# Performance work log

Hardware: AMD Instinct MI355X
Metric: run time of the kernel (lower is better)

The kernel has to match this reference:

```python
import jax, jax.numpy as jnp
import numpy as np

N_AGENTS = 3
OBS_DIM = 30
ACT_DIM = 9
HIDDEN = 128
HEADS = 4
HEAD_DIM = HIDDEN // HEADS
BATCH = 131072
NEG_SLOPE = 0.01
MASK_VAL = -1e10


def _leaky(x):
    return jnp.where(x >= 0, x, NEG_SLOPE * x)


def setup_inputs() -> dict:
    key = jax.random.key(0)
    ks = jax.random.split(key, 20)

    def init(k, shape, fan_in):
        return jax.random.normal(k, shape, dtype=jnp.float32) / np.sqrt(fan_in)

    inp = {
        "observations": jax.random.normal(ks[0], (BATCH, N_AGENTS, OBS_DIM), dtype=jnp.float32),
        "actions": jax.random.uniform(ks[1], (BATCH, N_AGENTS, ACT_DIM), dtype=jnp.float32),
        # per-agent embed weights, stacked over agents: [N, in, out] (already transposed vs torch)
        "W_o": init(ks[2], (N_AGENTS, OBS_DIM, HIDDEN), OBS_DIM),
        "b_o": jnp.zeros((N_AGENTS, HIDDEN), dtype=jnp.float32),
        "W_oa": init(ks[3], (N_AGENTS, OBS_DIM + ACT_DIM, HIDDEN), OBS_DIM + ACT_DIM),
        "b_oa": jnp.zeros((N_AGENTS, HIDDEN), dtype=jnp.float32),
        # shared attention projections: [in, out]
        "Wq": init(ks[4], (HIDDEN, HIDDEN), HIDDEN),
        "bq": jnp.zeros((HIDDEN,), dtype=jnp.float32),
        "Wk": init(ks[5], (HIDDEN, HIDDEN), HIDDEN),
        "bk": jnp.zeros((HIDDEN,), dtype=jnp.float32),
        "Wv": init(ks[6], (HIDDEN, HIDDEN), HIDDEN),
        "bv": jnp.zeros((HIDDEN,), dtype=jnp.float32),
        # per-agent critic MLP: Linear(2H->H) + LeakyReLU + Linear(H->A)
        "Wc1": init(ks[7], (N_AGENTS, 2 * HIDDEN, HIDDEN), 2 * HIDDEN),
        "bc1": jnp.zeros((N_AGENTS, HIDDEN), dtype=jnp.float32),
        "Wc2": init(ks[8], (N_AGENTS, HIDDEN, ACT_DIM), HIDDEN),
        "bc2": jnp.zeros((N_AGENTS, ACT_DIM), dtype=jnp.float32),
    }
    return inp


def reference(observations, actions, W_o, b_o, W_oa, b_oa, Wq, bq, Wk, bk, Wv, bv, Wc1, bc1, Wc2, bc2):
    B, N, _ = observations.shape

    # per-agent embeds as a single batched GEMM over the agent axis
    o_emb = _leaky(jnp.einsum('bnd,ndh->bnh', observations, W_o) + b_o)          # [B,N,H]
    oa = jnp.concatenate([observations, actions], axis=-1)                        # [B,N,O+A]
    oa_emb = _leaky(jnp.einsum('bnd,ndh->bnh', oa, W_oa) + b_oa)                  # [B,N,H]

    # shared Q/K/V projections, split heads -> [B, heads, N, head_dim]
    def heads(x):
        return x.reshape(B, N, HEADS, HEAD_DIM).transpose(0, 2, 1, 3)

    Q = heads(o_emb @ Wq + bq)
    K = heads(oa_emb @ Wk + bk)
    V = heads(oa_emb @ Wv + bv)

    scores = jnp.einsum('bhnd,bhmd->bhnm', Q, K) / np.sqrt(HEAD_DIM).astype(np.float32)
    mask = jnp.where(jnp.eye(N, dtype=bool), jnp.float32(MASK_VAL), 0.0)          # diag masked
    attn = jax.nn.softmax(scores + mask, axis=-1)
    attn_out = jnp.einsum('bhnm,bhmd->bhnd', attn, V)
    attn_out = attn_out.transpose(0, 2, 1, 3).reshape(B, N, HIDDEN)               # [B,N,H]

    # per-agent critics, again batched over the agent axis
    c_in = jnp.concatenate([o_emb, attn_out], axis=-1)                            # [B,N,2H]
    h = _leaky(jnp.einsum('bnd,ndh->bnh', c_in, Wc1) + bc1)
    q_values = jnp.einsum('bnh,nha->bna', h, Wc2) + bc2                           # [B,N,A]
    return q_values
```

## Files before the change

kernel.cpp:

```cpp
#include <hip/hip_runtime.h>
#include <stdint.h>

typedef unsigned short u16;
typedef unsigned int u32;
typedef __attribute__((ext_vector_type(8))) short short8;
typedef __attribute__((ext_vector_type(4))) float floatx4;

#define BATCH   131072
#define NA      3
#define OBS     30
#define ACTD    9
#define HID     128
#define HEADS   4
#define HD      32
#define MB      16
#define ROWS    (MB*NA)
#define LDC     136
#define LDOA    72
#define QSCALE  0.17677669529663687f
#define NTHREADS 512

#define OFF_WO    0
#define OFF_WOA   12288
#define OFF_WQ    36864
#define OFF_WK    53248
#define OFF_WV    69632
#define OFF_WC1   86016
#define OFF_WC2   184320
#define PRE_TOTAL 190464

__device__ __forceinline__ u16 f2bf(float f) {
    union { float f; u32 u; } v; v.f = f;
    return (u16)((v.u + 0x8000u) >> 16);
}
__device__ __forceinline__ u32 pk_bf16(float a, float b) {
    union { float f; u32 u; } x, y; x.f = a; y.f = b;
    return ((x.u + 0x8000u) >> 16) | ((y.u + 0x8000u) & 0xffff0000u);
}
__device__ __forceinline__ float lo16f(u32 w) { union { u32 u; float f; } v; v.u = w << 16; return v.f; }
__device__ __forceinline__ float hi16f(u32 w) { union { u32 u; float f; } v; v.u = w & 0xffff0000u; return v.f; }
__device__ __forceinline__ float leaky(float x) { return x >= 0.f ? x : 0.01f * x; }

__global__ void prepack_kernel(const float* __restrict__ Wo,  const float* __restrict__ Woa,
                               const float* __restrict__ Wq,  const float* __restrict__ Wk,
                               const float* __restrict__ Wv,  const float* __restrict__ Wc1,
                               const float* __restrict__ Wc2, u16* __restrict__ out) {
    int i = blockIdx.x * blockDim.x + threadIdx.x;
    if (i >= PRE_TOTAL) return;
    const float* src; int K, KT, perA, base, Nsrc, Nlim; float scl = 1.f;
    if (i < OFF_WOA)      { src = Wo;  K = 30;  KT = 1; perA = 4096;  base = OFF_WO;  Nsrc = 128; Nlim = 128; }
    else if (i < OFF_WQ)  { src = Woa; K = 39;  KT = 2; perA = 8192;  base = OFF_WOA; Nsrc = 128; Nlim = 128; }
    else if (i < OFF_WK)  { src = Wq;  K = 128; KT = 4; perA = 16384; base = OFF_WQ;  Nsrc = 128; Nlim = 128; scl = QSCALE; }
    else if (i < OFF_WV)  { src = Wk;  K = 128; KT = 4; perA = 16384; base = OFF_WK;  Nsrc = 128; Nlim = 128; }
    else if (i < OFF_WC1) { src = Wv;  K = 128; KT = 4; perA = 16384; base = OFF_WV;  Nsrc = 128; Nlim = 128; }
    else if (i < OFF_WC2) { src = Wc1; K = 256; KT = 8; perA = 32768; base = OFF_WC1; Nsrc = 128; Nlim = 128; }
    else                  { src = Wc2; K = 128; KT = 4; perA = 2048;  base = OFF_WC2; Nsrc = 9;   Nlim = 9;   }
    int j = i - base;
    int agent = j / perA;
    int r = j - agent * perA;
    int e = r & 7, lane = (r >> 3) & 63, fk = r >> 9;
    int kt = fk % KT, nt = fk / KT;
    int n = nt * 16 + (lane & 15);
    int k = kt * 32 + (lane >> 4) * 8 + e;
    u16 v = 0;
    if (k < K && n < Nlim) v = f2bf(src[(agent * K + k) * Nsrc + n] * scl);
    out[i] = v;
}

__global__ __launch_bounds__(NTHREADS, 6) void fused_kernel(
    const float* __restrict__ obs, const float* __restrict__ act,
    const float* __restrict__ b_o, const float* __restrict__ b_oa,
    const float* __restrict__ bq,  const float* __restrict__ bk_, const float* __restrict__ bv,
    const float* __restrict__ bc1, const float* __restrict__ bc2,
    const u16* __restrict__ pre, float* __restrict__ out)
{
    __shared__ __align__(16) u16 s_mem[4 * ROWS * LDC];
    u16* s_oemb  = s_mem;
    u16* s_oaemb = s_mem + ROWS * LDC;
    u16* s_bufA  = s_mem + 2 * ROWS * LDC;
    u16* s_bufB  = s_mem + 3 * ROWS * LDC;

    const int tid  = threadIdx.x;
    const int wave = tid >> 6, lane = tid & 63;
    const int l15  = lane & 15, quad = lane >> 4;
    const int b0   = blockIdx.x * MB;
    const short8* preV = (const short8*)pre;

    for (int g = tid; g < ROWS * 15; g += NTHREADS) {
        int r = g / 15, s = g - r * 15;
        int n = r / MB, bl = r - n * MB;
        const float* src = &obs[((b0 + bl) * NA + n) * OBS + 2 * s];
        *(u32*)&s_bufA[n * (MB * LDOA) + bl * LDOA + 2 * s] = pk_bf16(src[0], src[1]);
    }
    for (int g = tid; g < ROWS * 5; g += NTHREADS) {
        int r = g / 5, s = g - r * 5;
        int n = r / MB, bl = r - n * MB;
        const float* src = &act[((b0 + bl) * NA + n) * ACTD + 2 * s];
        float v0 = src[0], v1 = (s < 4) ? src[1] : 0.f;
        *(u32*)&s_bufA[n * (MB * LDOA) + bl * LDOA + 30 + 2 * s] = pk_bf16(v0, v1);
    }
    for (int g = tid; g < ROWS * 12; g += NTHREADS) {
        int r = g / 12, s = g - r * 12;
        int n = r / MB, bl = r - n * MB;
        *(u32*)&s_bufA[n * (MB * LDOA) + bl * LDOA + 40 + 2 * s] = 0;
    }
    __syncthreads();

    for (int sj = wave; sj < 24; sj += 8) {
        int osel = sj / 12;
        int rem = sj % 12, agent = rem >> 2, nh2 = rem & 3;
        int KTn = osel ? 2 : 1;
        const float* bias = osel ? b_oa : b_o;
        int preBase = osel ? (OFF_WOA / 8 + agent * 1024) : (OFF_WO / 8 + agent * 512);
        floatx4 acc[2] = {};
        for (int kt = 0; kt < KTn; kt++) {
            short8 a = *(const short8*)&s_bufA[agent * (MB * LDOA) + l15 * LDOA + kt * 32 + quad * 8];
            #pragma unroll
            for (int n2 = 0; n2 < 2; n2++) {
                int nt = nh2 * 2 + n2;
                short8 b = preV[preBase + (nt * KTn + kt) * 64 + lane];
                acc[n2] = __builtin_amdgcn_mfma_f32_16x16x32_bf16(a, b, acc[n2], 0, 0, 0);
            }
        }
        u16* dst = osel ? s_oaemb : s_oemb;
        #pragma unroll
        for (int n2 = 0; n2 < 2; n2++) {
            int col = (nh2 * 2 + n2) * 16 + l15;
            float bb = bias[agent * HID + col];
            #pragma unroll
            for (int rg = 0; rg < 4; rg++) {
                int m = quad * 4 + rg;
                dst[(m * NA + agent) * LDC + col] = f2bf(leaky(acc[n2][rg] + bb));
            }
        }
    }
    __syncthreads();

    {
        int proj = wave >> 2, nh2 = wave & 3;
        const u16* Abuf = proj ? s_oaemb : s_oemb;
        int preBase = (proj ? OFF_WK : OFF_WQ) / 8;
        u16* dst = proj ? s_bufB : s_bufA;
        const float* bias = proj ? bk_ : bq;
        float bscl = proj ? 1.f : QSCALE;
        short8 wf[8];
        #pragma unroll
        for (int n2 = 0; n2 < 2; n2++)
            #pragma unroll
            for (int kt = 0; kt < 4; kt++)
                wf[n2 * 4 + kt] = preV[preBase + ((nh2 * 2 + n2) * 4 + kt) * 64 + lane];
        for (int mt = 0; mt < 3; mt++) {
            short8 xa[4];
            #pragma unroll
            for (int kt = 0; kt < 4; kt++)
                xa[kt] = *(const short8*)&Abuf[(mt * 16 + l15) * LDC + kt * 32 + quad * 8];
            floatx4 acc[2] = {};
            #pragma unroll
            for (int n2 = 0; n2 < 2; n2++)
                #pragma unroll
                for (int kt = 0; kt < 4; kt++)
                    acc[n2] = __builtin_amdgcn_mfma_f32_16x16x32_bf16(xa[kt], wf[n2 * 4 + kt], acc[n2], 0, 0, 0);
            #pragma unroll
            for (int n2 = 0; n2 < 2; n2++) {
                int col = (nh2 * 2 + n2) * 16 + l15;
                float bb = bias[col] * bscl;
                #pragma unroll
                for (int rg = 0; rg < 4; rg++) {
                    int m = mt * 16 + quad * 4 + rg;
                    dst[m * LDC + col] = f2bf(acc[n2][rg] + bb);
                }
            }
        }
    }
    __syncthreads();

    float2 prob = make_float2(0.f, 0.f);
    int e3 = 0, h3 = 0, n3 = 0, m30 = 0, m31 = 0;
    const bool attn_thread = (tid < MB * HEADS * NA);
    if (attn_thread) {
        int r = tid;
        e3 = r / (HEADS * NA); r -= e3 * HEADS * NA; h3 = r / NA; n3 = r - h3 * NA;
        m30 = (n3 == 0) ? 1 : 0;
        m31 = (n3 == 2) ? 1 : 2;
        const uint4* qp  = (const uint4*)&s_bufA[(e3 * NA + n3) * LDC + h3 * HD];
        const uint4* kp0 = (const uint4*)&s_bufB[(e3 * NA + m30) * LDC + h3 * HD];
        const uint4* kp1 = (const uint4*)&s_bufB[(e3 * NA + m31) * LDC + h3 * HD];
        float s0 = 0.f, s1 = 0.f;
        #pragma unroll
        for (int c = 0; c < 4; c++) {
            uint4 qw = qp[c], aw = kp0[c], bw = kp1[c];
            u32 qv[4] = {qw.x, qw.y, qw.z, qw.w};
            u32 av[4] = {aw.x, aw.y, aw.z, aw.w};
            u32 bv_[4] = {bw.x, bw.y, bw.z, bw.w};
            #pragma unroll
            for (int j = 0; j < 4; j++) {
                float ql = lo16f(qv[j]), qh = hi16f(qv[j]);
                s0 += ql * lo16f(av[j]) + qh * hi16f(av[j]);
                s1 += ql * lo16f(bv_[j]) + qh * hi16f(bv_[j]);
            }
        }
        float mx = fmaxf(s0, s1);
        float p0 = __expf(s0 - mx), p1 = __expf(s1 - mx);
        float inv = 1.f / (p0 + p1);
        prob = make_float2(p0 * inv, p1 * inv);
    }
    __syncthreads();

    {
        int nt = wave;
        short8 wf[4];
        #pragma unroll
        for (int kt = 0; kt < 4; kt++)
            wf[kt] = preV[OFF_WV / 8 + (nt * 4 + kt) * 64 + lane];
        for (int mt = 0; mt < 3; mt++) {
            short8 xa[4];
            #pragma unroll
            for (int kt = 0; kt < 4; kt++)
                xa[kt] = *(const short8*)&s_oaemb[(mt * 16 + l15) * LDC + kt * 32 + quad * 8];
            floatx4 acc = {};
            #pragma unroll
            for (int kt = 0; kt < 4; kt++)
                acc = __builtin_amdgcn_mfma_f32_16x16x32_bf16(xa[kt], wf[kt], acc, 0, 0, 0);
            int col = nt * 16 + l15;
            float bb = bv[col];
            #pragma unroll
            for (int rg = 0; rg < 4; rg++) {
                int m = mt * 16 + quad * 4 + rg;
                s_bufA[m * LDC + col] = f2bf(acc[rg] + bb);
            }
        }
    }
    __syncthreads();

    if (attn_thread) {
        const uint4* v0p = (const uint4*)&s_bufA[(e3 * NA + m30) * LDC + h3 * HD];
        const uint4* v1p = (const uint4*)&s_bufA[(e3 * NA + m31) * LDC + h3 * HD];
        uint4* dst = (uint4*)&s_oaemb[(e3 * NA + n3) * LDC + h3 * HD];
        #pragma unroll
        for (int c = 0; c < 4; c++) {
            uint4 aw = v0p[c], bw = v1p[c], ow;
            u32 av[4] = {aw.x, aw.y, aw.z, aw.w};
            u32 bv_[4] = {bw.x, bw.y, bw.z, bw.w};
            u32 ov[4];
            #pragma unroll
            for (int j = 0; j < 4; j++) {
                float lo = prob.x * lo16f(av[j]) + prob.y * lo16f(bv_[j]);
                float hi = prob.x * hi16f(av[j]) + prob.y * hi16f(bv_[j]);
                ov[j] = pk_bf16(lo, hi);
            }
            ow.x = ov[0]; ow.y = ov[1]; ow.z = ov[2]; ow.w = ov[3];
            dst[c] = ow;
        }
    }
    __syncthreads();

    for (int sj = wave; sj < 24; sj += 8) {
        int agent = sj >> 3, nt = sj & 7;
        floatx4 acc = {};
        for (int kt = 0; kt < 8; kt++) {
            const u16* A = (kt < 4) ? s_oemb : s_oaemb;
            int kk = (kt & 3) * 32 + quad * 8;
            short8 a = *(const short8*)&A[(l15 * NA + agent) * LDC + kk];
            short8 b = preV[OFF_WC1 / 8 + agent * 4096 + (nt * 8 + kt) * 64 + lane];
            acc = __builtin_amdgcn_mfma_f32_16x16x32_bf16(a, b, acc, 0, 0, 0);
        }
        int col = nt * 16 + l15;
        float bb = bc1[agent * HID + col];
        #pragma unroll
        for (int rg = 0; rg < 4; rg++) {
            int m = quad * 4 + rg;
            s_bufB[(m * NA + agent) * LDC + col] = f2bf(leaky(acc[rg] + bb));
        }
    }
    __syncthreads();

    if (wave < NA) {
        int agent = wave;
        floatx4 acc = {};
        #pragma unroll
        for (int kt = 0; kt < 4; kt++) {
            short8 a = *(const short8*)&s_bufB[(l15 * NA + agent) * LDC + kt * 32 + quad * 8];
            short8 b = preV[OFF_WC2 / 8 + agent * 256 + kt * 64 + lane];
            acc = __builtin_amdgcn_mfma_f32_16x16x32_bf16(a, b, acc, 0, 0, 0);
        }
        int col = l15;
        if (col < ACTD) {
            float bb = bc2[agent * ACTD + col];
            #pragma unroll
            for (int rg = 0; rg < 4; rg++) {
                int m = quad * 4 + rg;
                out[((b0 + m) * NA + agent) * ACTD + col] = acc[rg] + bb;
            }
        }
    }
}

extern "C" void kernel_launch(void* const* d_in, const int* in_sizes, int n_in,
                              void* d_out, int out_size, void* d_ws, size_t ws_size,
                              hipStream_t stream) {
    const float* obs = (const float*)d_in[0];
    const float* act = (const float*)d_in[1];
    const float* Wo  = (const float*)d_in[2];
    const float* bo  = (const float*)d_in[3];
    const float* Woa = (const float*)d_in[4];
    const float* boa = (const float*)d_in[5];
    const float* Wq  = (const float*)d_in[6];
    const float* bq  = (const float*)d_in[7];
    const float* Wk  = (const float*)d_in[8];
    const float* bk  = (const float*)d_in[9];
    const float* Wv  = (const float*)d_in[10];
    const float* bv  = (const float*)d_in[11];
    const float* Wc1 = (const float*)d_in[12];
    const float* bc1 = (const float*)d_in[13];
    const float* Wc2 = (const float*)d_in[14];
    const float* bc2 = (const float*)d_in[15];
    u16* pre = (u16*)d_ws;

    prepack_kernel<<<(PRE_TOTAL + 255) / 256, 256, 0, stream>>>(Wo, Woa, Wq, Wk, Wv, Wc1, Wc2, pre);
    fused_kernel<<<BATCH / MB, NTHREADS, 0, stream>>>(obs, act, bo, boa, bq, bk, bv, bc1, bc2, pre,
                                                      (float*)d_out);
}
```

Measured before the change: 261.6 us.

## Prefetch weight fragments into registers ahead of each GEMM stage

Global loads of the per-stage bf16 weight fragments and biases are hoisted ahead of earlier stages and barriers (embed and Q/K weights at kernel start, V weights after input staging, Wc1 after the Q/K projection, Wc2 before the critic layer). This hides global-memory latency behind the LDS staging and preceding compute. The zero-fill loop also switches to 16-byte stores. The cost is much higher register pressure, e.g. 24 short8 for Wc1 alone held across stages, which can lower occupancy or cause spills at 512 threads per block.

```diff
diff --git a/kernel.cpp b/kernel.cpp
--- a/kernel.cpp
+++ b/kernel.cpp
@@ -86,6 +86,40 @@
     const int b0   = blockIdx.x * MB;
     const short8* preV = (const short8*)pre;
 
+    short8 w1[3][2][2]; float b1v[3][2];
+    int os1[3], ag1[3], nh21[3], ktn1[3];
+    #pragma unroll
+    for (int j = 0; j < 3; j++) {
+        int sj = wave + 8 * j;
+        int osel = sj / 12;
+        int rem = sj % 12, agent = rem >> 2, nh2 = rem & 3;
+        int KTn = osel ? 2 : 1;
+        int preBase = osel ? (OFF_WOA / 8 + agent * 1024) : (OFF_WO / 8 + agent * 512);
+        const float* bias = osel ? b_oa : b_o;
+        os1[j] = osel; ag1[j] = agent; nh21[j] = nh2; ktn1[j] = KTn;
+        #pragma unroll
+        for (int n2 = 0; n2 < 2; n2++) {
+            int nt = nh2 * 2 + n2;
+            w1[j][n2][0] = preV[preBase + (nt * KTn + 0) * 64 + lane];
+            if (KTn == 2) w1[j][n2][1] = preV[preBase + (nt * KTn + 1) * 64 + lane];
+            b1v[j][n2] = bias[agent * HID + nt * 16 + l15];
+        }
+    }
+    short8 w2[8]; float b2v[2];
+    {
+        int proj = wave >> 2, nh2s = wave & 3;
+        int preBase = (proj ? OFF_WK : OFF_WQ) / 8;
+        const float* bias = proj ? bk_ : bq;
+        float bscl = proj ? 1.f : QSCALE;
+        #pragma unroll
+        for (int n2 = 0; n2 < 2; n2++) {
+            b2v[n2] = bias[(nh2s * 2 + n2) * 16 + l15] * bscl;
+            #pragma unroll
+            for (int kt = 0; kt < 4; kt++)
+                w2[n2 * 4 + kt] = preV[preBase + ((nh2s * 2 + n2) * 4 + kt) * 64 + lane];
+        }
+    }
+
     for (int g = tid; g < ROWS * 15; g += NTHREADS) {
         int r = g / 15, s = g - r * 15;
         int n = r / MB, bl = r - n * MB;
@@ -99,34 +133,38 @@
         float v0 = src[0], v1 = (s < 4) ? src[1] : 0.f;
         *(u32*)&s_bufA[n * (MB * LDOA) + bl * LDOA + 30 + 2 * s] = pk_bf16(v0, v1);
     }
-    for (int g = tid; g < ROWS * 12; g += NTHREADS) {
-        int r = g / 12, s = g - r * 12;
+    for (int g = tid; g < ROWS * 3; g += NTHREADS) {
+        int r = g / 3, s = g - r * 3;
         int n = r / MB, bl = r - n * MB;
-        *(u32*)&s_bufA[n * (MB * LDOA) + bl * LDOA + 40 + 2 * s] = 0;
-    }
-    __syncthreads();
-
-    for (int sj = wave; sj < 24; sj += 8) {
-        int osel = sj / 12;
-        int rem = sj % 12, agent = rem >> 2, nh2 = rem & 3;
-        int KTn = osel ? 2 : 1;
-        const float* bias = osel ? b_oa : b_o;
-        int preBase = osel ? (OFF_WOA / 8 + agent * 1024) : (OFF_WO / 8 + agent * 512);
+        *(uint4*)&s_bufA[n * (MB * LDOA) + bl * LDOA + 40 + 8 * s] = make_uint4(0, 0, 0, 0);
+    }
+    __syncthreads();
+
+    short8 w3[4]; float b3v;
+    {
+        #pragma unroll
+        for (int kt = 0; kt < 4; kt++)
+            w3[kt] = preV[OFF_WV / 8 + (wave * 4 + kt) * 64 + lane];
+        b3v = bv[wave * 16 + l15];
+    }
+
+    #pragma unroll
+    for (int j = 0; j < 3; j++) {
+        int osel = os1[j], agent = ag1[j], nh2 = nh21[j], KTn = ktn1[j];
         floatx4 acc[2] = {};
-        for (int kt = 0; kt < KTn; kt++) {
-            short8 a = *(const short8*)&s_bufA[agent * (MB * LDOA) + l15 * LDOA + kt * 32 + quad * 8];
-            #pragma unroll
-            for (int n2 = 0; n2 < 2; n2++) {
-                int nt = nh2 * 2 + n2;
-                short8 b = preV[preBase + (nt * KTn + kt) * 64 + lane];
-                acc[n2] = __builtin_amdgcn_mfma_f32_16x16x32_bf16(a, b, acc[n2], 0, 0, 0);
+        #pragma unroll
+        for (int kt = 0; kt < 2; kt++) {
+            if (kt < KTn) {
+                short8 a = *(const short8*)&s_bufA[agent * (MB * LDOA) + l15 * LDOA + kt * 32 + quad * 8];
+                acc[0] = __builtin_amdgcn_mfma_f32_16x16x32_bf16(a, w1[j][0][kt], acc[0], 0, 0, 0);
+                acc[1] = __builtin_amdgcn_mfma_f32_16x16x32_bf16(a, w1[j][1][kt], acc[1], 0, 0, 0);
             }
         }
         u16* dst = osel ? s_oaemb : s_oemb;
         #pragma unroll
         for (int n2 = 0; n2 < 2; n2++) {
             int col = (nh2 * 2 + n2) * 16 + l15;
-            float bb = bias[agent * HID + col];
+            float bb = b1v[j][n2];
             #pragma unroll
             for (int rg = 0; rg < 4; rg++) {
                 int m = quad * 4 + rg;
@@ -139,16 +177,7 @@
     {
         int proj = wave >> 2, nh2 = wave & 3;
         const u16* Abuf = proj ? s_oaemb : s_oemb;
-        int preBase = (proj ? OFF_WK : OFF_WQ) / 8;
         u16* dst = proj ? s_bufB : s_bufA;
-        const float* bias = proj ? bk_ : bq;
-        float bscl = proj ? 1.f : QSCALE;
-        short8 wf[8];
-        #pragma unroll
-        for (int n2 = 0; n2 < 2; n2++)
-            #pragma unroll
-            for (int kt = 0; kt < 4; kt++)
-                wf[n2 * 4 + kt] = preV[preBase + ((nh2 * 2 + n2) * 4 + kt) * 64 + lane];
         for (int mt = 0; mt < 3; mt++) {
             short8 xa[4];
             #pragma unroll
@@ -159,11 +188,11 @@
             for (int n2 = 0; n2 < 2; n2++)
                 #pragma unroll
                 for (int kt = 0; kt < 4; kt++)
-                    acc[n2] = __builtin_amdgcn_mfma_f32_16x16x32_bf16(xa[kt], wf[n2 * 4 + kt], acc[n2], 0, 0, 0);
+                    acc[n2] = __builtin_amdgcn_mfma_f32_16x16x32_bf16(xa[kt], w2[n2 * 4 + kt], acc[n2], 0, 0, 0);
             #pragma unroll
             for (int n2 = 0; n2 < 2; n2++) {
                 int col = (nh2 * 2 + n2) * 16 + l15;
-                float bb = bias[col] * bscl;
+                float bb = b2v[n2];
                 #pragma unroll
                 for (int rg = 0; rg < 4; rg++) {
                     int m = mt * 16 + quad * 4 + rg;
@@ -173,6 +202,15 @@
         }
     }
     __syncthreads();
+
+    short8 w4[3][8]; float b4v[3];
+    #pragma unroll
+    for (int j = 0; j < 3; j++) {
+        #pragma unroll
+        for (int kt = 0; kt < 8; kt++)
+            w4[j][kt] = preV[OFF_WC1 / 8 + j * 4096 + (wave * 8 + kt) * 64 + lane];
+        b4v[j] = bc1[j * HID + wave * 16 + l15];
+    }
 
     float2 prob = make_float2(0.f, 0.f);
     int e3 = 0, h3 = 0, n3 = 0, m30 = 0, m31 = 0;
@@ -208,10 +246,6 @@
 
     {
         int nt = wave;
-        short8 wf[4];
-        #pragma unroll
-        for (int kt = 0; kt < 4; kt++)
-            wf[kt] = preV[OFF_WV / 8 + (nt * 4 + kt) * 64 + lane];
         for (int mt = 0; mt < 3; mt++) {
             short8 xa[4];
             #pragma unroll
@@ -220,9 +254,9 @@
             floatx4 acc = {};
             #pragma unroll
             for (int kt = 0; kt < 4; kt++)
-                acc = __builtin_amdgcn_mfma_f32_16x16x32_bf16(xa[kt], wf[kt], acc, 0, 0, 0);
+                acc = __builtin_amdgcn_mfma_f32_16x16x32_bf16(xa[kt], w3[kt], acc, 0, 0, 0);
             int col = nt * 16 + l15;
-            float bb = bv[col];
+            float bb = b3v;
             #pragma unroll
             for (int rg = 0; rg < 4; rg++) {
                 int m = mt * 16 + quad * 4 + rg;
@@ -254,18 +288,27 @@
     }
     __syncthreads();
 
-    for (int sj = wave; sj < 24; sj += 8) {
-        int agent = sj >> 3, nt = sj & 7;
+    short8 w5[4]; float b5v = 0.f;
+    if (wave < NA) {
+        #pragma unroll
+        for (int kt = 0; kt < 4; kt++)
+            w5[kt] = preV[OFF_WC2 / 8 + wave * 256 + kt * 64 + lane];
+        if (l15 < ACTD) b5v = bc2[wave * ACTD + l15];
+    }
+
+    #pragma unroll
+    for (int j = 0; j < 3; j++) {
+        int agent = j, nt = wave;
         floatx4 acc = {};
+        #pragma unroll
         for (int kt = 0; kt < 8; kt++) {
             const u16* A = (kt < 4) ? s_oemb : s_oaemb;
             int kk = (kt & 3) * 32 + quad * 8;
             short8 a = *(const short8*)&A[(l15 * NA + agent) * LDC + kk];
-            short8 b = preV[OFF_WC1 / 8 + agent * 4096 + (nt * 8 + kt) * 64 + lane];
-            acc = __builtin_amdgcn_mfma_f32_16x16x32_bf16(a, b, acc, 0, 0, 0);
+            acc = __builtin_amdgcn_mfma_f32_16x16x32_bf16(a, w4[j][kt], acc, 0, 0, 0);
         }
         int col = nt * 16 + l15;
-        float bb = bc1[agent * HID + col];
+        float bb = b4v[j];
         #pragma unroll
         for (int rg = 0; rg < 4; rg++) {
             int m = quad * 4 + rg;
@@ -280,16 +323,14 @@
         #pragma unroll
         for (int kt = 0; kt < 4; kt++) {
             short8 a = *(const short8*)&s_bufB[(l15 * NA + agent) * LDC + kt * 32 + quad * 8];
-            short8 b = preV[OFF_WC2 / 8 + agent * 256 + kt * 64 + lane];
-            acc = __builtin_amdgcn_mfma_f32_16x16x32_bf16(a, b, acc, 0, 0, 0);
+            acc = __builtin_amdgcn_mfma_f32_16x16x32_bf16(a, w5[kt], acc, 0, 0, 0);
         }
         int col = l15;
         if (col < ACTD) {
-            float bb = bc2[agent * ACTD + col];
             #pragma unroll
             for (int rg = 0; rg < 4; rg++) {
                 int m = quad * 4 + rg;
-                out[((b0 + m) * NA + agent) * ACTD + col] = acc[rg] + bb;
+                out[((b0 + m) * NA + agent) * ACTD + col] = acc[rg] + b5v;
             }
         }
     }
```

Result: slower. 897.4 us (+243.0%).

## Prefetch all stage weights into registers ahead of each barrier phase

Applied to the files above, without the earlier changes.

Weight and bias fragments for every GEMM stage (embeds, Q/K, V, critic layer 1, critic layer 2) are now loaded from global memory into registers one phase early, so their latency overlaps the input staging, the attention math and the barrier waits. The embedding and critic stages are restructured with a fixed per-wave assignment, so each wave handles its three jobs with the weights already in hand. The padding-zero fill also switches to 16-byte stores. The cost is much higher register pressure, mostly from the 24 short8 critic weight fragments, which may lower occupancy or cause spills.

```diff
diff --git a/kernel.cpp b/kernel.cpp
--- a/kernel.cpp
+++ b/kernel.cpp
@@ -28,6 +28,8 @@
 #define OFF_WC1   86016
 #define OFF_WC2   184320
 #define PRE_TOTAL 190464
+
+#define MFMA(A,B,C) __builtin_amdgcn_mfma_f32_16x16x32_bf16((A),(B),(C),0,0,0)
 
 __device__ __forceinline__ u16 f2bf(float f) {
     union { float f; u32 u; } v; v.f = f;
@@ -86,6 +88,49 @@
     const int b0   = blockIdx.x * MB;
     const short8* preV = (const short8*)pre;
 
+    const int nh2 = wave & 3;
+
+    const int ag0 = wave >> 2;
+    const int ag2 = (wave + 4) >> 2;
+    const int pb0 = OFF_WO / 8 + ag0 * 512;
+    const int pb1 = (wave < 4) ? (OFF_WO / 8 + 2 * 512) : (OFF_WOA / 8);
+    const int kt1n = (wave < 4) ? 1 : 2;
+    const int pb2 = OFF_WOA / 8 + ag2 * 1024;
+    short8 w1_00 = preV[pb0 + (nh2 * 2 + 0) * 64 + lane];
+    short8 w1_01 = preV[pb0 + (nh2 * 2 + 1) * 64 + lane];
+    short8 w1_100 = preV[pb1 + ((nh2 * 2 + 0) * kt1n + 0) * 64 + lane];
+    short8 w1_101 = preV[pb1 + ((nh2 * 2 + 0) * kt1n + 1) * 64 + lane];
+    short8 w1_110 = preV[pb1 + ((nh2 * 2 + 1) * kt1n + 0) * 64 + lane];
+    short8 w1_111 = preV[pb1 + ((nh2 * 2 + 1) * kt1n + 1) * 64 + lane];
+    short8 w1_200 = preV[pb2 + ((nh2 * 2 + 0) * 2 + 0) * 64 + lane];
+    short8 w1_201 = preV[pb2 + ((nh2 * 2 + 0) * 2 + 1) * 64 + lane];
+    short8 w1_210 = preV[pb2 + ((nh2 * 2 + 1) * 2 + 0) * 64 + lane];
+    short8 w1_211 = preV[pb2 + ((nh2 * 2 + 1) * 2 + 1) * 64 + lane];
+    const float* bj0 = b_o + ag0 * HID;
+    const float* bj1 = (wave < 4) ? (b_o + 2 * HID) : b_oa;
+    const float* bj2 = b_oa + ag2 * HID;
+    float b1_00 = bj0[(nh2 * 2 + 0) * 16 + l15];
+    float b1_01 = bj0[(nh2 * 2 + 1) * 16 + l15];
+    float b1_10 = bj1[(nh2 * 2 + 0) * 16 + l15];
+    float b1_11 = bj1[(nh2 * 2 + 1) * 16 + l15];
+    float b1_20 = bj2[(nh2 * 2 + 0) * 16 + l15];
+    float b1_21 = bj2[(nh2 * 2 + 1) * 16 + l15];
+
+    const int proj = wave >> 2;
+    const int pbqk = (proj ? OFF_WK : OFF_WQ) / 8;
+    const float* bqk = proj ? bk_ : bq;
+    const float bscl = proj ? 1.f : QSCALE;
+    short8 w2_00 = preV[pbqk + ((nh2 * 2 + 0) * 4 + 0) * 64 + lane];
+    short8 w2_01 = preV[pbqk + ((nh2 * 2 + 0) * 4 + 1) * 64 + lane];
+    short8 w2_02 = preV[pbqk + ((nh2 * 2 + 0) * 4 + 2) * 64 + lane];
+    short8 w2_03 = preV[pbqk + ((nh2 * 2 + 0) * 4 + 3) * 64 + lane];
+    short8 w2_10 = preV[pbqk + ((nh2 * 2 + 1) * 4 + 0) * 64 + lane];
+    short8 w2_11 = preV[pbqk + ((nh2 * 2 + 1) * 4 + 1) * 64 + lane];
+    short8 w2_12 = preV[pbqk + ((nh2 * 2 + 1) * 4 + 2) * 64 + lane];
+    short8 w2_13 = preV[pbqk + ((nh2 * 2 + 1) * 4 + 3) * 64 + lane];
+    float b2_0 = bqk[(nh2 * 2 + 0) * 16 + l15] * bscl;
+    float b2_1 = bqk[(nh2 * 2 + 1) * 16 + l15] * bscl;
+
     for (int g = tid; g < ROWS * 15; g += NTHREADS) {
         int r = g / 15, s = g - r * 15;
         int n = r / MB, bl = r - n * MB;
@@ -99,80 +144,121 @@
         float v0 = src[0], v1 = (s < 4) ? src[1] : 0.f;
         *(u32*)&s_bufA[n * (MB * LDOA) + bl * LDOA + 30 + 2 * s] = pk_bf16(v0, v1);
     }
-    for (int g = tid; g < ROWS * 12; g += NTHREADS) {
-        int r = g / 12, s = g - r * 12;
+    for (int g = tid; g < ROWS * 3; g += NTHREADS) {
+        int r = g / 3, s = g - r * 3;
         int n = r / MB, bl = r - n * MB;
-        *(u32*)&s_bufA[n * (MB * LDOA) + bl * LDOA + 40 + 2 * s] = 0;
-    }
-    __syncthreads();
-
-    for (int sj = wave; sj < 24; sj += 8) {
-        int osel = sj / 12;
-        int rem = sj % 12, agent = rem >> 2, nh2 = rem & 3;
-        int KTn = osel ? 2 : 1;
-        const float* bias = osel ? b_oa : b_o;
-        int preBase = osel ? (OFF_WOA / 8 + agent * 1024) : (OFF_WO / 8 + agent * 512);
-        floatx4 acc[2] = {};
-        for (int kt = 0; kt < KTn; kt++) {
-            short8 a = *(const short8*)&s_bufA[agent * (MB * LDOA) + l15 * LDOA + kt * 32 + quad * 8];
-            #pragma unroll
-            for (int n2 = 0; n2 < 2; n2++) {
-                int nt = nh2 * 2 + n2;
-                short8 b = preV[preBase + (nt * KTn + kt) * 64 + lane];
-                acc[n2] = __builtin_amdgcn_mfma_f32_16x16x32_bf16(a, b, acc[n2], 0, 0, 0);
-            }
-        }
-        u16* dst = osel ? s_oaemb : s_oemb;
+        *(uint4*)&s_bufA[n * (MB * LDOA) + bl * LDOA + 40 + 8 * s] = make_uint4(0, 0, 0, 0);
+    }
+    __syncthreads();
+
+    short8 w3_0 = preV[OFF_WV / 8 + (wave * 4 + 0) * 64 + lane];
+    short8 w3_1 = preV[OFF_WV / 8 + (wave * 4 + 1) * 64 + lane];
+    short8 w3_2 = preV[OFF_WV / 8 + (wave * 4 + 2) * 64 + lane];
+    short8 w3_3 = preV[OFF_WV / 8 + (wave * 4 + 3) * 64 + lane];
+    float b3v = bv[wave * 16 + l15];
+
+    {
+        short8 a = *(const short8*)&s_bufA[ag0 * (MB * LDOA) + l15 * LDOA + quad * 8];
+        floatx4 acc0 = {}, acc1 = {};
+        acc0 = MFMA(a, w1_00, acc0);
+        acc1 = MFMA(a, w1_01, acc1);
+        int col0 = nh2 * 32 + l15;
         #pragma unroll
-        for (int n2 = 0; n2 < 2; n2++) {
-            int col = (nh2 * 2 + n2) * 16 + l15;
-            float bb = bias[agent * HID + col];
-            #pragma unroll
-            for (int rg = 0; rg < 4; rg++) {
-                int m = quad * 4 + rg;
-                dst[(m * NA + agent) * LDC + col] = f2bf(leaky(acc[n2][rg] + bb));
-            }
-        }
-    }
-    __syncthreads();
-
-    {
-        int proj = wave >> 2, nh2 = wave & 3;
+        for (int rg = 0; rg < 4; rg++) {
+            int m = quad * 4 + rg;
+            s_oemb[(m * NA + ag0) * LDC + col0]      = f2bf(leaky(acc0[rg] + b1_00));
+            s_oemb[(m * NA + ag0) * LDC + col0 + 16] = f2bf(leaky(acc1[rg] + b1_01));
+        }
+    }
+    {
+        int ag1 = (wave < 4) ? 2 : 0;
+        short8 a0 = *(const short8*)&s_bufA[ag1 * (MB * LDOA) + l15 * LDOA + quad * 8];
+        floatx4 acc0 = {}, acc1 = {};
+        acc0 = MFMA(a0, w1_100, acc0);
+        acc1 = MFMA(a0, w1_110, acc1);
+        if (wave >= 4) {
+            short8 a1 = *(const short8*)&s_bufA[ag1 * (MB * LDOA) + l15 * LDOA + 32 + quad * 8];
+            acc0 = MFMA(a1, w1_101, acc0);
+            acc1 = MFMA(a1, w1_111, acc1);
+        }
+        u16* dst = (wave < 4) ? s_oemb : s_oaemb;
+        int col0 = nh2 * 32 + l15;
+        #pragma unroll
+        for (int rg = 0; rg < 4; rg++) {
+            int m = quad * 4 + rg;
+            dst[(m * NA + ag1) * LDC + col0]      = f2bf(leaky(acc0[rg] + b1_10));
+            dst[(m * NA + ag1) * LDC + col0 + 16] = f2bf(leaky(acc1[rg] + b1_11));
+        }
+    }
+    {
+        short8 a0 = *(const short8*)&s_bufA[ag2 * (MB * LDOA) + l15 * LDOA + quad * 8];
+        short8 a1 = *(const short8*)&s_bufA[ag2 * (MB * LDOA) + l15 * LDOA + 32 + quad * 8];
+        floatx4 acc0 = {}, acc1 = {};
+        acc0 = MFMA(a0, w1_200, acc0);
+        acc0 = MFMA(a1, w1_201, acc0);
+        acc1 = MFMA(a0, w1_210, acc1);
+        acc1 = MFMA(a1, w1_211, acc1);
+        int col0 = nh2 * 32 + l15;
+        #pragma unroll
+        for (int rg = 0; rg < 4; rg++) {
+            int m = quad * 4 + rg;
+            s_oaemb[(m * NA + ag2) * LDC + col0]      = f2bf(leaky(acc0[rg] + b1_20));
+            s_oaemb[(m * NA + ag2) * LDC + col0 + 16] = f2bf(leaky(acc1[rg] + b1_21));
+        }
+    }
+    __syncthreads();
+
+    {
         const u16* Abuf = proj ? s_oaemb : s_oemb;
-        int preBase = (proj ? OFF_WK : OFF_WQ) / 8;
         u16* dst = proj ? s_bufB : s_bufA;
-        const float* bias = proj ? bk_ : bq;
-        float bscl = proj ? 1.f : QSCALE;
-        short8 wf[8];
-        #pragma unroll
-        for (int n2 = 0; n2 < 2; n2++)
-            #pragma unroll
-            for (int kt = 0; kt < 4; kt++)
-                wf[n2 * 4 + kt] = preV[preBase + ((nh2 * 2 + n2) * 4 + kt) * 64 + lane];
+        int col0 = nh2 * 32 + l15;
         for (int mt = 0; mt < 3; mt++) {
-            short8 xa[4];
-            #pragma unroll
-            for (int kt = 0; kt < 4; kt++)
-                xa[kt] = *(const short8*)&Abuf[(mt * 16 + l15) * LDC + kt * 32 + quad * 8];
-            floatx4 acc[2] = {};
-            #pragma unroll
-            for (int n2 = 0; n2 < 2; n2++)
-                #pragma unroll
-                for (int kt = 0; kt < 4; kt++)
-                    acc[n2] = __builtin_amdgcn_mfma_f32_16x16x32_bf16(xa[kt], wf[n2 * 4 + kt], acc[n2], 0, 0, 0);
-            #pragma unroll
-            for (int n2 = 0; n2 < 2; n2++) {
-                int col = (nh2 * 2 + n2) * 16 + l15;
-                float bb = bias[col] * bscl;
-                #pragma unroll
-                for (int rg = 0; rg < 4; rg++) {
-                    int m = mt * 16 + quad * 4 + rg;
-                    dst[m * LDC + col] = f2bf(acc[n2][rg] + bb);
-                }
-            }
-        }
-    }
-    __syncthreads();
+            short8 xa0 = *(const short8*)&Abuf[(mt * 16 + l15) * LDC + 0  + quad * 8];
+            short8 xa1 = *(const short8*)&Abuf[(mt * 16 + l15) * LDC + 32 + quad * 8];
+            short8 xa2 = *(const short8*)&Abuf[(mt * 16 + l15) * LDC + 64 + quad * 8];
+            short8 xa3 = *(const short8*)&Abuf[(mt * 16 + l15) * LDC + 96 + quad * 8];
+            floatx4 acc0 = {}, acc1 = {};
+            acc0 = MFMA(xa0, w2_00, acc0); acc0 = MFMA(xa1, w2_01, acc0);
+            acc0 = MFMA(xa2, w2_02, acc0); acc0 = MFMA(xa3, w2_03, acc0);
+            acc1 = MFMA(xa0, w2_10, acc1); acc1 = MFMA(xa1, w2_11, acc1);
+            acc1 = MFMA(xa2, w2_12, acc1); acc1 = MFMA(xa3, w2_13, acc1);
+            #pragma unroll
+            for (int rg = 0; rg < 4; rg++) {
+                int m = mt * 16 + quad * 4 + rg;
+                dst[m * LDC + col0]      = f2bf(acc0[rg] + b2_0);
+                dst[m * LDC + col0 + 16] = f2bf(acc1[rg] + b2_1);
+            }
+        }
+    }
+    __syncthreads();
+
+    short8 w4_00 = preV[OFF_WC1 / 8 + 0 * 4096 + (wave * 8 + 0) * 64 + lane];
+    short8 w4_01 = preV[OFF_WC1 / 8 + 0 * 4096 + (wave * 8 + 1) * 64 + lane];
+    short8 w4_02 = preV[OFF_WC1 / 8 + 0 * 4096 + (wave * 8 + 2) * 64 + lane];
+    short8 w4_03 = preV[OFF_WC1 / 8 + 0 * 4096 + (wave * 8 + 3) * 64 + lane];
+    short8 w4_04 = preV[OFF_WC1 / 8 + 0 * 4096 + (wave * 8 + 4) * 64 + lane];
+    short8 w4_05 = preV[OFF_WC1 / 8 + 0 * 4096 + (wave * 8 + 5) * 64 + lane];
+    short8 w4_06 = preV[OFF_WC1 / 8 + 0 * 4096 + (wave * 8 + 6) * 64 + lane];
+    short8 w4_07 = preV[OFF_WC1 / 8 + 0 * 4096 + (wave * 8 + 7) * 64 + lane];
+    short8 w4_10 = preV[OFF_WC1 / 8 + 1 * 4096 + (wave * 8 + 0) * 64 + lane];
+    short8 w4_11 = preV[OFF_WC1 / 8 + 1 * 4096 + (wave * 8 + 1) * 64 + lane];
+    short8 w4_12 = preV[OFF_WC1 / 8 + 1 * 4096 + (wave * 8 + 2) * 64 + lane];
+    short8 w4_13 = preV[OFF_WC1 / 8 + 1 * 4096 + (wave * 8 + 3) * 64 + lane];
+    short8 w4_14 = preV[OFF_WC1 / 8 + 1 * 4096 + (wave * 8 + 4) * 64 + lane];
+    short8 w4_15 = preV[OFF_WC1 / 8 + 1 * 4096 + (wave * 8 + 5) * 64 + lane];
+    short8 w4_16 = preV[OFF_WC1 / 8 + 1 * 4096 + (wave * 8 + 6) * 64 + lane];
+    short8 w4_17 = preV[OFF_WC1 / 8 + 1 * 4096 + (wave * 8 + 7) * 64 + lane];
+    short8 w4_20 = preV[OFF_WC1 / 8 + 2 * 4096 + (wave * 8 + 0) * 64 + lane];
+    short8 w4_21 = preV[OFF_WC1 / 8 + 2 * 4096 + (wave * 8 + 1) * 64 + lane];
+    short8 w4_22 = preV[OFF_WC1 / 8 + 2 * 4096 + (wave * 8 + 2) * 64 + lane];
+    short8 w4_23 = preV[OFF_WC1 / 8 + 2 * 4096 + (wave * 8 + 3) * 64 + lane];
+    short8 w4_24 = preV[OFF_WC1 / 8 + 2 * 4096 + (wave * 8 + 4) * 64 + lane];
+    short8 w4_25 = preV[OFF_WC1 / 8 + 2 * 4096 + (wave * 8 + 5) * 64 + lane];
+    short8 w4_26 = preV[OFF_WC1 / 8 + 2 * 4096 + (wave * 8 + 6) * 64 + lane];
+    short8 w4_27 = preV[OFF_WC1 / 8 + 2 * 4096 + (wave * 8 + 7) * 64 + lane];
+    float b4_0 = bc1[0 * HID + wave * 16 + l15];
+    float b4_1 = bc1[1 * HID + wave * 16 + l15];
+    float b4_2 = bc1[2 * HID + wave * 16 + l15];
 
     float2 prob = make_float2(0.f, 0.f);
     int e3 = 0, h3 = 0, n3 = 0, m30 = 0, m31 = 0;
@@ -207,26 +293,19 @@
     __syncthreads();
 
     {
-        int nt = wave;
-        short8 wf[4];
-        #pragma unroll
-        for (int kt = 0; kt < 4; kt++)
-            wf[kt] = preV[OFF_WV / 8 + (nt * 4 + kt) * 64 + lane];
+        int colv = wave * 16 + l15;
         for (int mt = 0; mt < 3; mt++) {
-            short8 xa[4];
-            #pragma unroll
-            for (int kt = 0; kt < 4; kt++)
-                xa[kt] = *(const short8*)&s_oaemb[(mt * 16 + l15) * LDC + kt * 32 + quad * 8];
+            short8 xa0 = *(const short8*)&s_oaemb[(mt * 16 + l15) * LDC + 0  + quad * 8];
+            short8 xa1 = *(const short8*)&s_oaemb[(mt * 16 + l15) * LDC + 32 + quad * 8];
+            short8 xa2 = *(const short8*)&s_oaemb[(mt * 16 + l15) * LDC + 64 + quad * 8];
+            short8 xa3 = *(const short8*)&s_oaemb[(mt * 16 + l15) * LDC + 96 + quad * 8];
             floatx4 acc = {};
-            #pragma unroll
-            for (int kt = 0; kt < 4; kt++)
-                acc = __builtin_amdgcn_mfma_f32_16x16x32_bf16(xa[kt], wf[kt], acc, 0, 0, 0);
-            int col = nt * 16 + l15;
-            float bb = bv[col];
+            acc = MFMA(xa0, w3_0, acc); acc = MFMA(xa1, w3_1, acc);
+            acc = MFMA(xa2, w3_2, acc); acc = MFMA(xa3, w3_3, acc);
             #pragma unroll
             for (int rg = 0; rg < 4; rg++) {
                 int m = mt * 16 + quad * 4 + rg;
-                s_bufA[m * LDC + col] = f2bf(acc[rg] + bb);
+                s_bufA[m * LDC + colv] = f2bf(acc[rg] + b3v);
             }
         }
     }
@@ -254,22 +333,65 @@
     }
     __syncthreads();
 
-    for (int sj = wave; sj < 24; sj += 8) {
-        int agent = sj >> 3, nt = sj & 7;
-        floatx4 acc = {};
-        for (int kt = 0; kt < 8; kt++) {
-            const u16* A = (kt < 4) ? s_oemb : s_oaemb;
-            int kk = (kt & 3) * 32 + quad * 8;
-            short8 a = *(const short8*)&A[(l15 * NA + agent) * LDC + kk];
-            short8 b = preV[OFF_WC1 / 8 + agent * 4096 + (nt * 8 + kt) * 64 + lane];
-            acc = __builtin_amdgcn_mfma_f32_16x16x32_bf16(a, b, acc, 0, 0, 0);
-        }
-        int col = nt * 16 + l15;
-        float bb = bc1[agent * HID + col];
-        #pragma unroll
-        for (int rg = 0; rg < 4; rg++) {
-            int m = quad * 4 + rg;
-            s_bufB[(m * NA + agent) * LDC + col] = f2bf(leaky(acc[rg] + bb));
+    const int w5a = (wave < NA) ? wave : 0;
+    short8 w5_0 = preV[OFF_WC2 / 8 + w5a * 256 + 0 * 64 + lane];
+    short8 w5_1 = preV[OFF_WC2 / 8 + w5a * 256 + 1 * 64 + lane];
+    short8 w5_2 = preV[OFF_WC2 / 8 + w5a * 256 + 2 * 64 + lane];
+    short8 w5_3 = preV[OFF_WC2 / 8 + w5a * 256 + 3 * 64 + lane];
+    float b5v = bc2[w5a * ACTD + ((l15 < ACTD) ? l15 : 0)];
+
+    {
+        int colc = wave * 16 + l15;
+        {
+            floatx4 acc = {};
+            short8 a;
+            a = *(const short8*)&s_oemb [(l15 * NA + 0) * LDC + 0  + quad * 8]; acc = MFMA(a, w4_00, acc);
+            a = *(const short8*)&s_oemb [(l15 * NA + 0) * LDC + 32 + quad * 8]; acc = MFMA(a, w4_01, acc);
+            a = *(const short8*)&s_oemb [(l15 * NA + 0) * LDC + 64 + quad * 8]; acc = MFMA(a, w4_02, acc);
+            a = *(const short8*)&s_oemb [(l15 * NA + 0) * LDC + 96 + quad * 8]; acc = MFMA(a, w4_03, acc);
+            a = *(const short8*)&s_oaemb[(l15 * NA + 0) * LDC + 0  + quad * 8]; acc = MFMA(a, w4_04, acc);
+            a = *(const short8*)&s_oaemb[(l15 * NA + 0) * LDC + 32 + quad * 8]; acc = MFMA(a, w4_05, acc);
+            a = *(const short8*)&s_oaemb[(l15 * NA + 0) * LDC + 64 + quad * 8]; acc = MFMA(a, w4_06, acc);
+            a = *(const short8*)&s_oaemb[(l15 * NA + 0) * LDC + 96 + quad * 8]; acc = MFMA(a, w4_07, acc);
+            #pragma unroll
+            for (int rg = 0; rg < 4; rg++) {
+                int m = quad * 4 + rg;
+                s_bufB[(m * NA + 0) * LDC + colc] = f2bf(leaky(acc[rg] + b4_0));
+            }
+        }
+        {
+            floatx4 acc = {};
+            short8 a;
+            a = *(const short8*)&s_oemb [(l15 * NA + 1) * LDC + 0  + quad * 8]; acc = MFMA(a, w4_10, acc);
+            a = *(const short8*)&s_oemb [(l15 * NA + 1) * LDC + 32 + quad * 8]; acc = MFMA(a, w4_11, acc);
+            a = *(const short8*)&s_oemb [(l15 * NA + 1) * LDC + 64 + quad * 8]; acc = MFMA(a, w4_12, acc);
+            a = *(const short8*)&s_oemb [(l15 * NA + 1) * LDC + 96 + quad * 8]; acc = MFMA(a, w4_13, acc);
+            a = *(const short8*)&s_oaemb[(l15 * NA + 1) * LDC + 0  + quad * 8]; acc = MFMA(a, w4_14, acc);
+            a = *(const short8*)&s_oaemb[(l15 * NA + 1) * LDC + 32 + quad * 8]; acc = MFMA(a, w4_15, acc);
+            a = *(const short8*)&s_oaemb[(l15 * NA + 1) * LDC + 64 + quad * 8]; acc = MFMA(a, w4_16, acc);
+            a = *(const short8*)&s_oaemb[(l15 * NA + 1) * LDC + 96 + quad * 8]; acc = MFMA(a, w4_17, acc);
+            #pragma unroll
+            for (int rg = 0; rg < 4; rg++) {
+                int m = quad * 4 + rg;
+                s_bufB[(m * NA + 1) * LDC + colc] = f2bf(leaky(acc[rg] + b4_1));
+            }
+        }
+        {
+            floatx4 acc = {};
+            short8 a;
+            a = *(const short8*)&s_oemb [(l15 * NA + 2) * LDC + 0  + quad * 8]; acc = MFMA(a, w4_20, acc);
+            a = *(const short8*)&s_oemb [(l15 * NA + 2) * LDC + 32 + quad * 8]; acc = MFMA(a, w4_21, acc);
+            a = *(const short8*)&s_oemb [(l15 * NA + 2) * LDC + 64 + quad * 8]; acc = MFMA(a, w4_22, acc);
+            a = *(const short8*)&s_oemb [(l15 * NA + 2) * LDC + 96 + quad * 8]; acc = MFMA(a, w4_23, acc);
+            a = *(const short8*)&s_oaemb[(l15 * NA + 2) * LDC + 0  + quad * 8]; acc = MFMA(a, w4_24, acc);
+            a = *(const short8*)&s_oaemb[(l15 * NA + 2) * LDC + 32 + quad * 8]; acc = MFMA(a, w4_25, acc);
+            a = *(const short8*)&s_oaemb[(l15 * NA + 2) * LDC + 64 + quad * 8]; acc = MFMA(a, w4_26, acc);
+            a = *(const short8*)&s_oaemb[(l15 * NA + 2) * LDC + 96 + quad * 8]; acc = MFMA(a, w4_27, acc);
+            #pragma unroll
+            for (int rg = 0; rg < 4; rg++) {
+                int m = quad * 4 + rg;
+                s_bufB[(m * NA + 2) * LDC + colc] = f2bf(leaky(acc[rg] + b4_2));
+            }
         }
     }
     __syncthreads();
@@ -277,19 +399,16 @@
     if (wave < NA) {
         int agent = wave;
         floatx4 acc = {};
-        #pragma unroll
-        for (int kt = 0; kt < 4; kt++) {
-            short8 a = *(const short8*)&s_bufB[(l15 * NA + agent) * LDC + kt * 32 + quad * 8];
-            short8 b = preV[OFF_WC2 / 8 + agent * 256 + kt * 64 + lane];
-            acc = __builtin_amdgcn_mfma_f32_16x16x32_bf16(a, b, acc, 0, 0, 0);
-        }
-        int col = l15;
-        if (col < ACTD) {
-            float bb = bc2[agent * ACTD + col];
+        short8 a;
+        a = *(const short8*)&s_bufB[(l15 * NA + agent) * LDC + 0  + quad * 8]; acc = MFMA(a, w5_0, acc);
+        a = *(const short8*)&s_bufB[(l15 * NA + agent) * LDC + 32 + quad * 8]; acc = MFMA(a, w5_1, acc);
+        a = *(const short8*)&s_bufB[(l15 * NA + agent) * LDC + 64 + quad * 8]; acc = MFMA(a, w5_2, acc);
+        a = *(const short8*)&s_bufB[(l15 * NA + agent) * LDC + 96 + quad * 8]; acc = MFMA(a, w5_3, acc);
+        if (l15 < ACTD) {
             #pragma unroll
             for (int rg = 0; rg < 4; rg++) {
                 int m = quad * 4 + rg;
-                out[((b0 + m) * NA + agent) * ACTD + col] = acc[rg] + bb;
+                out[((b0 + m) * NA + agent) * ACTD + l15] = acc[rg] + b5v;
             }
         }
     }
```

After: 873.0 us. 234% more time.
